# Kernel optimization log

Measured on AMD Instinct MI355X. Metric: run time of the kernel, lower is better.

## Reference

```python
import jax, jax.numpy as jnp
import numpy as np

EPS_BN = 1e-5


def conv2d(x, w, b=None, pad=0, groups=1):
    y = jax.lax.conv_general_dilated(
        x, w, window_strides=(1, 1), padding=[(pad, pad), (pad, pad)],
        dimension_numbers=('NCHW', 'OIHW', 'NCHW'), feature_group_count=groups)
    if b is not None:
        y = y + b[None, :, None, None]
    return y


def bilinear_sample(x, py, px):
    # x: (C,H,W); py,px: (T,Ho,Wo) fractional sample coords. Zero outside borders
    # (matches torchvision deform_conv2d per-corner masking).
    C, H, W = x.shape
    xf = x.reshape(C, -1)
    y0 = jnp.floor(py)
    x0 = jnp.floor(px)

    def g(yi, xi):
        valid = (yi >= 0) & (yi <= H - 1) & (xi >= 0) & (xi <= W - 1)
        idx = (jnp.clip(yi, 0, H - 1).astype(jnp.int32) * W
               + jnp.clip(xi, 0, W - 1).astype(jnp.int32))
        v = xf[:, idx.reshape(-1)].reshape((C,) + idx.shape)  # (C,T,Ho,Wo)
        return jnp.where(valid[None], v, 0.0)

    wy1 = py - y0
    wx1 = px - x0
    wy0 = 1.0 - wy1
    wx0 = 1.0 - wx1
    return (g(y0, x0) * (wy0 * wx0)[None]
            + g(y0, x0 + 1.0) * (wy0 * wx1)[None]
            + g(y0 + 1.0, x0) * (wy1 * wx0)[None]
            + g(y0 + 1.0, x0 + 1.0) * (wy1 * wx1)[None])


def deform_depthwise(x, offset, dyn_w, k):
    # x: (B,C,H,W); offset: (B,2*k*k,H,W) interleaved (dy,dx) per tap;
    # dyn_w: (B,C,k,k) per-sample depthwise kernels. stride=1, pad=k//2.
    B, C, H, W = x.shape
    T = k * k
    pad = k // 2
    off = offset.reshape(B, T, 2, H, W)
    ky, kx = jnp.meshgrid(jnp.arange(k), jnp.arange(k), indexing='ij')
    base_y = (jnp.arange(H)[None, :, None] - pad
              + ky.reshape(T)[:, None, None]).astype(x.dtype)  # (T,H,1)
    base_x = (jnp.arange(W)[None, None, :] - pad
              + kx.reshape(T)[:, None, None]).astype(x.dtype)  # (T,1,W)
    py = base_y[None] + off[:, :, 0]  # (B,T,H,W)
    px = base_x[None] + off[:, :, 1]
    v = jax.vmap(bilinear_sample)(x, py, px)  # (B,C,T,H,W)
    return jnp.einsum('bct,bcthw->bchw', dyn_w.reshape(B, C, T), v)


def reference(F_c, dec_w, dec_b, off1_w, off1_b, off2_w, off2_b,
              akg_dw_w, akg_head_w, akg_head_b, pw2_w, pw2_b,
              bn_gamma, bn_beta):
    k = 3
    Kd = 7
    B, C, H, W = F_c.shape
    R = dec_w.shape[0]

    # TargetRegionDecoupler: F_i = F * M_i + F
    M = jax.nn.softmax(conv2d(F_c, dec_w, dec_b), axis=1)  # (B,R,H,W)

    outs = []
    for i in range(R):
        F_i = F_c * (1.0 + M[:, i:i + 1])
        # OffsetGenerator
        h = jax.nn.relu(conv2d(F_i, off1_w[i], off1_b[i], pad=1))
        p_i = conv2d(h, off2_w[i], off2_b[i], pad=1)  # (B,2*k*k,H,W)
        # AdaptiveKernelGenerator (exact adaptive pool: 56 -> 7 via 8x8 mean)
        d = F_i.reshape(B, C, Kd, H // Kd, Kd, W // Kd).mean(axis=(3, 5))
        d = jax.nn.relu(conv2d(d, akg_dw_w[i], None, pad=1, groups=C))
        d = d.mean(axis=(2, 3), keepdims=True)  # AdaptiveAvgPool2d(1)
        K_i = jnp.tanh(conv2d(d, akg_head_w[i], akg_head_b[i]).reshape(B, C, k, k))
        # per-sample dynamic depthwise deformable conv
        outs.append(deform_depthwise(F_i, p_i, K_i, k))

    O = conv2d(jnp.concatenate(outs, axis=1), pw2_w, pw2_b)
    # BatchNorm2d, training-mode batch statistics
    mean = O.mean(axis=(0, 2, 3), keepdims=True)
    var = O.var(axis=(0, 2, 3), keepdims=True)
    O = (O - mean) * jax.lax.rsqrt(var + EPS_BN)
    O = O * bn_gamma[None, :, None, None] + bn_beta[None, :, None, None]
    return O


def setup_inputs() -> dict:
    key = jax.random.key(0)
    ks = jax.random.split(key, 10)
    B, C, H, W = 8, 256, 56, 56
    k, R = 3, 2
    hid = max(32, C // 4)
    return {
        'F_c': jax.random.normal(ks[0], (B, C, H, W), jnp.float32),
        'dec_w': jax.random.normal(ks[1], (R, C, 1, 1), jnp.float32) * 0.1,
        'dec_b': jnp.zeros((R,), jnp.float32),
        'off1_w': jax.random.normal(ks[2], (R, hid, C, 3, 3), jnp.float32) * 0.05,
        'off1_b': jnp.zeros((R, hid), jnp.float32),
        'off2_w': jax.random.normal(ks[3], (R, 2 * k * k, hid, 3, 3), jnp.float32) * 0.01,
        'off2_b': jnp.zeros((R, 2 * k * k), jnp.float32),
        'akg_dw_w': jax.random.normal(ks[4], (R, C, 1, 3, 3), jnp.float32) * 0.1,
        'akg_head_w': jax.random.normal(ks[5], (R, C * k * k, C, 1, 1), jnp.float32) * 0.05,
        'akg_head_b': jnp.zeros((R, C * k * k), jnp.float32),
        'pw2_w': jax.random.normal(ks[6], (C, R * C, 1, 1), jnp.float32) * 0.05,
        'pw2_b': jnp.zeros((C,), jnp.float32),
        'bn_gamma': jnp.ones((C,), jnp.float32),
        'bn_beta': jnp.zeros((C,), jnp.float32),
    }
```

## Files before the change

### kernel.cpp

```cpp
#include <hip/hip_runtime.h>
#include <hip/hip_bf16.h>

#define BB 8
#define CC_ 256
#define HH 56
#define WW 56
#define HWSZ (HH*WW)
#define RR_ 2
#define HID 64
#define FPR ((size_t)8*58*58*256)
#define HPR ((size_t)8*58*58*64)
#define NPIX ((size_t)BB*HWSZ)

typedef __hip_bfloat16 bf16;
typedef __attribute__((ext_vector_type(8))) short short8;
typedef __attribute__((ext_vector_type(4))) short short4_t;
typedef __attribute__((ext_vector_type(4))) float f32x4;

struct Tap { int o00, o01, o10, o11; float w00, w01, w10, w11; };

__device__ __forceinline__ float b2f(bf16 v){ return __bfloat162float(v); }
__device__ __forceinline__ bf16 f2b(float v){ return __float2bfloat16(v); }
__device__ __forceinline__ float bs2f(short s){ return __uint_as_float(((unsigned)(unsigned short)s)<<16); }

__global__ __launch_bounds__(256) void k_scalepack(const float* __restrict__ F, const float* __restrict__ dec_w,
                                                   const float* __restrict__ dec_b,
                                                   bf16* __restrict__ Fp, float* __restrict__ rowsum){
    __shared__ float lds_f[256][57];
    __shared__ float lw0[256], lw1[256];
    __shared__ float ls0[56], ls1[56];
    int bx = blockIdx.x; int b = bx/HH, gy = bx%HH;
    int tid = threadIdx.x;
    lw0[tid] = dec_w[tid]; lw1[tid] = dec_w[CC_+tid];
    const float* Fb = F + (size_t)b*CC_*HWSZ + gy*WW;
    for (int it = 0; it < 56; ++it){
        int idx = it*256 + tid;
        int c = idx / 56, x = idx - c*56;
        lds_f[c][x] = Fb[(size_t)c*HWSZ + x];
    }
    __syncthreads();
    if (tid < 56){
        float a0 = dec_b[0], a1 = dec_b[1];
        for (int c = 0; c < CC_; ++c){ float v = lds_f[c][tid]; a0 += v*lw0[c]; a1 += v*lw1[c]; }
        float m = fmaxf(a0,a1);
        float e0 = __expf(a0-m), e1 = __expf(a1-m);
        float inv = 1.0f/(e0+e1);
        ls0[tid] = 1.0f + e0*inv; ls1[tid] = 1.0f + e1*inv;
    }
    __syncthreads();
    bf16 z = f2b(0.f);
    for (int r = 0; r < 2; ++r){
        const float* lsr = r ? ls1 : ls0;
        bf16* slab = Fp + (size_t)r*FPR + (size_t)b*58*58*256;
        bf16* dst = slab + ((size_t)(gy+1)*58 + 1)*256 + tid;
        for (int x2 = 0; x2 < 56; ++x2) dst[(size_t)x2*256] = f2b(lds_f[tid][x2] * lsr[x2]);
        float* rs = rowsum + ((((size_t)(r*8+b)*56 + gy)*7))*256 + tid;
        #pragma unroll
        for (int v = 0; v < 7; ++v){
            float sum = 0.f;
            #pragma unroll
            for (int k = 0; k < 8; ++k) sum += lds_f[tid][v*8+k] * lsr[v*8+k];
            rs[(size_t)v*256] = sum;
        }
        bf16* rowp = slab + (size_t)(gy+1)*58*256;
        rowp[tid] = z;
        rowp[57*256 + tid] = z;
        if (gy == 0){ for (int cidx = 0; cidx < 58; ++cidx) slab[(size_t)cidx*256 + tid] = z; }
        if (gy == 55){ bf16* r57 = slab + (size_t)57*58*256;
                       for (int cidx = 0; cidx < 58; ++cidx) r57[(size_t)cidx*256 + tid] = z; }
    }
}

__global__ void k_bprep_all(const float* __restrict__ w1, const float* __restrict__ wpw,
                            const float* __restrict__ wc2,
                            bf16* __restrict__ Bp, bf16* __restrict__ Bpw, bf16* __restrict__ Bc){
    int id = blockIdx.x;
    int L = threadIdx.x;
    if (id < 576){
        int nt = id & 3; id >>= 2; int icc = id & 7; id >>= 3; int t = id % 9; int r = id / 9;
        int oc = nt*16 + (L&15);
        const float* wr = w1 + (size_t)r*HID*CC_*9;
        bf16* out = Bp + (((((size_t)r*9 + t)*8 + icc)*4 + nt)*64 + L)*8;
        #pragma unroll
        for (int j = 0; j < 8; ++j){
            int ic = icc*32 + (L>>4)*8 + j;
            out[j] = f2b(wr[((size_t)oc*CC_ + ic)*9 + t]);
        }
    } else if (id < 832){
        id -= 576;
        int kk = id >> 4, nt = id & 15;
        int oc = nt*16 + (L&15);
        bf16* out = Bpw + (((size_t)(kk*16+nt))*64 + L)*8;
        #pragma unroll
        for (int j = 0; j < 8; ++j){
            int ic = kk*32 + (L>>4)*8 + j;
            out[j] = f2b(wpw[(size_t)oc*512 + ic]);
        }
    } else {
        id -= 832;
        int nt = id & 1; id >>= 1; int ks = id % 18; int r = id / 18;
        int t = ks >> 1, chunk = ks & 1;
        int oc = nt*16 + (L&15);
        const float* wr = wc2 + (size_t)r*18*HID*9;
        bf16* out = Bc + ((((size_t)r*18 + ks)*2 + nt)*64 + L)*8;
        #pragma unroll
        for (int j = 0; j < 8; ++j){
            int ic = chunk*32 + (L>>4)*8 + j;
            out[j] = (oc < 18) ? f2b(wr[((size_t)oc*HID + ic)*9 + t]) : f2b(0.f);
        }
    }
}

__global__ __launch_bounds__(256, 1) void k_conv1(const bf16* __restrict__ Fp, const bf16* __restrict__ Bp,
                                                  const float* __restrict__ bias, bf16* __restrict__ hp){
    __shared__ __attribute__((aligned(16))) bf16 alds[4*58*264];
    __shared__ __attribute__((aligned(16))) bf16 blds[16384];
    int bx = blockIdx.x;
    int x8 = bx & 7, g = bx >> 3;
    int r = x8 >> 2;
    int b = (g/28)*4 + (x8 & 3);
    int yp = g % 28;
    int y0 = yp*2;
    int tid = threadIdx.x; int wave = tid>>6, lane = tid&63;
    int m = lane&15, q = lane>>4;
    int x0 = (wave==3) ? 40 : wave*16;
    f32x4 acc[2][4];
    #pragma unroll
    for (int i=0;i<2;++i)
        #pragma unroll
        for (int j=0;j<4;++j) acc[i][j] = (f32x4){0,0,0,0};
    const bf16* Fb = Fp + (size_t)r*FPR + ((size_t)b*58*58)*256;
    const bf16* Bpr = Bp + (size_t)r*9*16384;
    short8 pf[8];
    #pragma unroll
    for (int j = 0; j < 8; ++j) pf[j] = *(const short8*)(Bpr + (size_t)(j*256 + tid)*8);
    const bf16* FbA = Fb + (size_t)y0*58*256;
    for (int kb = 0; kb < 4; ++kb){
        short8 v[8];
        #pragma unroll
        for (int j = 0; j < 8; ++j){
            int k = kb*8 + j;
            if (k < 29) v[j] = *(const short8*)(FbA + (size_t)k*2048 + tid*8);
        }
        #pragma unroll
        for (int j = 0; j < 8; ++j){
            int k = kb*8 + j;
            if (k < 29){
                int e = k*2048 + tid*8;
                int xl = e >> 8, c = e & 255;
                int row = xl / 58, x = xl - row*58;
                *(short8*)&alds[row*15312 + x*264 + c] = v[j];
            }
        }
    }
    #pragma unroll 1
    for (int t = 0; t < 9; ++t){
        __syncthreads();
        #pragma unroll
        for (int j = 0; j < 8; ++j) *(short8*)&blds[(j*256 + tid)*8] = pf[j];
        __syncthreads();
        if (t < 8){
            const bf16* src = Bpr + (size_t)(t+1)*16384;
            #pragma unroll
            for (int j = 0; j < 8; ++j) pf[j] = *(const short8*)(src + (size_t)(j*256 + tid)*8);
        }
        int ty = t/3, tx = t%3;
        int abase = ty*15312 + (x0+m+tx)*264 + q*8;
        #pragma unroll
        for (int icc = 0; icc < 8; ++icc){
            short8 a0 = *(const short8*)&alds[abase + icc*32];
            short8 a1 = *(const short8*)&alds[abase + 15312 + icc*32];
            const bf16* bb = &blds[icc*2048 + lane*8];
            short8 b0 = *(const short8*)(bb);
            short8 b1 = *(const short8*)(bb + 512);
            short8 b2 = *(const short8*)(bb + 1024);
            short8 b3 = *(const short8*)(bb + 1536);
            acc[0][0] = __builtin_amdgcn_mfma_f32_16x16x32_bf16(a0, b0, acc[0][0], 0, 0, 0);
            acc[1][0] = __builtin_amdgcn_mfma_f32_16x16x32_bf16(a1, b0, acc[1][0], 0, 0, 0);
            acc[0][1] = __builtin_amdgcn_mfma_f32_16x16x32_bf16(a0, b1, acc[0][1], 0, 0, 0);
            acc[1][1] = __builtin_amdgcn_mfma_f32_16x16x32_bf16(a1, b1, acc[1][1], 0, 0, 0);
            acc[0][2] = __builtin_amdgcn_mfma_f32_16x16x32_bf16(a0, b2, acc[0][2], 0, 0, 0);
            acc[1][2] = __builtin_amdgcn_mfma_f32_16x16x32_bf16(a1, b2, acc[1][2], 0, 0, 0);
            acc[0][3] = __builtin_amdgcn_mfma_f32_16x16x32_bf16(a0, b3, acc[0][3], 0, 0, 0);
            acc[1][3] = __builtin_amdgcn_mfma_f32_16x16x32_bf16(a1, b3, acc[1][3], 0, 0, 0);
        }
    }
    const float* br = bias + r*HID;
    bf16* slab = hp + (size_t)r*HPR + (size_t)b*58*58*64;
    bf16 z = f2b(0.f);
    #pragma unroll
    for (int rr = 0; rr < 2; ++rr){
        int y = y0 + rr;
        bf16* hrow = slab + ((size_t)(y+1)*58 + 1)*64;
        #pragma unroll
        for (int nt = 0; nt < 4; ++nt){
            int oc = nt*16 + m;
            float bv = br[oc];
            #pragma unroll
            for (int r2 = 0; r2 < 4; ++r2){
                int x = x0 + q*4 + r2;
                hrow[(size_t)x*64 + oc] = f2b(fmaxf(acc[rr][nt][r2] + bv, 0.f));
            }
        }
        bf16* rowp = slab + (size_t)(y+1)*58*64;
        if (tid < 64) rowp[tid] = z;
        else if (tid < 128) rowp[57*64 + (tid-64)] = z;
        if (y == 0){ for (int idx = tid; idx < 58*64; idx += 256) slab[idx] = z; }
        if (y == 55){ bf16* r57 = slab + (size_t)57*58*64;
                      for (int idx = tid; idx < 58*64; idx += 256) r57[idx] = z; }
    }
}

__global__ __launch_bounds__(256) void k_conv2m(const bf16* __restrict__ hp, const bf16* __restrict__ Bc,
                                                const float* __restrict__ bias, Tap* __restrict__ tap){
    __shared__ float pld[18][56];
    int bx = blockIdx.x; int b = bx & 7; int rid = bx >> 3; int y = rid % 56; int r = rid / 56;
    int tid = threadIdx.x; int wave = tid>>6, lane = tid&63;
    int m = lane&15, q = lane>>4;
    int x0 = (wave==3) ? 40 : wave*16;
    f32x4 acc0 = {0,0,0,0}, acc1 = {0,0,0,0};
    const bf16* Hb = hp + (size_t)r*HPR + ((size_t)b*58 + y)*58*64;
    const bf16* Bcr = Bc + (size_t)r*18*2*64*8;
    #pragma unroll
    for (int t = 0; t < 9; ++t){
        int ty = t/3, tx = t%3;
        const bf16* arow = Hb + ((size_t)ty*58 + (x0+m+tx))*64 + q*8;
        #pragma unroll
        for (int chunk = 0; chunk < 2; ++chunk){
            short8 a = *(const short8*)(arow + chunk*32);
            const bf16* bb = Bcr + (((size_t)(t*2+chunk))*2*64 + lane)*8;
            short8 b0 = *(const short8*)(bb);
            short8 b1 = *(const short8*)(bb + 64*8);
            acc0 = __builtin_amdgcn_mfma_f32_16x16x32_bf16(a, b0, acc0, 0, 0, 0);
            acc1 = __builtin_amdgcn_mfma_f32_16x16x32_bf16(a, b1, acc1, 0, 0, 0);
        }
    }
    const float* br = bias + r*18;
    #pragma unroll
    for (int r2 = 0; r2 < 4; ++r2){
        int x = x0 + q*4 + r2;
        pld[m][x] = acc0[r2] + br[m];
        if (m < 2) pld[16+m][x] = acc1[r2] + br[16+m];
    }
    __syncthreads();
    for (int e = tid; e < 504; e += 256){
        int t = e / 56, x = e % 56;
        int ky = t / 3, kx = t % 3;
        float dy = pld[2*t][x];
        float dx = pld[2*t+1][x];
        float py = (float)(y - 1 + ky) + dy;
        float px = (float)(x - 1 + kx) + dx;
        float y0f = floorf(py), x0f = floorf(px);
        float wy1 = py - y0f, wx1 = px - x0f;
        float wy0 = 1.f - wy1, wx0 = 1.f - wx1;
        float vy0 = (y0f >= 0.f  && y0f <= 55.f) ? 1.f : 0.f;
        float vy1 = (y0f >= -1.f && y0f <= 54.f) ? 1.f : 0.f;
        float vx0 = (x0f >= 0.f  && x0f <= 55.f) ? 1.f : 0.f;
        float vx1 = (x0f >= -1.f && x0f <= 54.f) ? 1.f : 0.f;
        int yy0 = (int)y0f, x0i = (int)x0f;
        int iy0 = min(max(yy0,0),55),   iy1 = min(max(yy0+1,0),55);
        int ix0 = min(max(x0i,0),55),   ix1 = min(max(x0i+1,0),55);
        Tap td;
        td.o00 = ((iy0+1)*58 + ix0+1)*256;
        td.o01 = ((iy0+1)*58 + ix1+1)*256;
        td.o10 = ((iy1+1)*58 + ix0+1)*256;
        td.o11 = ((iy1+1)*58 + ix1+1)*256;
        td.w00 = wy0*wx0*vy0*vx0;
        td.w01 = wy0*wx1*vy0*vx1;
        td.w10 = wy1*wx0*vy1*vx0;
        td.w11 = wy1*wx1*vy1*vx1;
        size_t pid = ((size_t)(r*8 + b))*3136 + y*56 + x;
        tap[pid*9 + t] = td;
    }
}

__global__ __launch_bounds__(256) void k_akg_s(const float* __restrict__ rowsum, const float* __restrict__ dw,
                                               float* __restrict__ s){
    int rb = blockIdx.x; int r = rb >> 3;
    int c = threadIdx.x;
    const float* rs = rowsum + ((size_t)rb*56*7)*256 + c;
    float d[7][7];
    #pragma unroll
    for (int u = 0; u < 7; ++u)
        #pragma unroll
        for (int v = 0; v < 7; ++v){
            float acc = 0.f;
            #pragma unroll
            for (int k = 0; k < 8; ++k) acc += rs[(size_t)((u*8+k)*7 + v)*256];
            d[u][v] = acc * (1.f/64.f);
        }
    const float* wp = dw + (size_t)r*CC_*9 + c*9;
    float w[9];
    #pragma unroll
    for (int k = 0; k < 9; ++k) w[k] = wp[k];
    float tot = 0.f;
    #pragma unroll
    for (int u = 0; u < 7; ++u)
        #pragma unroll
        for (int v = 0; v < 7; ++v){
            float acc = 0.f;
            #pragma unroll
            for (int ky = 0; ky < 3; ++ky){
                int uu = u+ky-1; if ((unsigned)uu >= 7u) continue;
                #pragma unroll
                for (int kx = 0; kx < 3; ++kx){
                    int vv = v+kx-1; if ((unsigned)vv >= 7u) continue;
                    acc += d[uu][vv]*w[ky*3+kx];
                }
            }
            tot += fmaxf(acc, 0.f);
        }
    s[(size_t)rb*CC_ + c] = tot * (1.f/49.f);
}

__global__ void k_akg_head(const float* __restrict__ s, const float* __restrict__ hw,
                           const float* __restrict__ hb, float* __restrict__ Kw){
    int gid = blockIdx.x; int r = gid / 72; int id = gid % 72;
    int b = id / 9; int og = id % 9;
    __shared__ float sv[CC_];
    int tid = threadIdx.x;
    sv[tid] = s[(size_t)(r*8+b)*CC_ + tid];
    __syncthreads();
    int o = og*256 + tid;
    const float* wp = hw + (size_t)r*2304*CC_ + (size_t)o*CC_;
    float acc = hb[(size_t)r*2304 + o];
    for (int c2=0;c2<CC_;++c2) acc += wp[c2]*sv[c2];
    int c = o / 9, t = o - 9*c;
    Kw[((size_t)r*BB + b)*2304 + t*256 + c] = tanhf(acc);
}

__global__ __launch_bounds__(256, 8) void k_deform(const bf16* __restrict__ Fp, const Tap* __restrict__ tap,
                                                   const float* __restrict__ Kw, bf16* __restrict__ outsN){
    __shared__ float klds[2432];
    __shared__ Tap tlds[4][18];
    int bx = blockIdx.x; int b = bx & 7; int rest = bx >> 3;
    int pg = rest % 392; int creg = rest / 392;
    int tid = threadIdx.x; int w = tid >> 6, l = tid & 63;
    int wu = __builtin_amdgcn_readfirstlane(w);
    int yx0 = pg*8 + wu*2;
    size_t slab = (size_t)(creg*8 + b)*3136;
    const float* Kb = Kw + ((size_t)creg*8 + b)*2304;
    for (int i = tid*4; i < 2304; i += 1024){
        f32x4 v = *(const f32x4*)(Kb + i);
        int t = i >> 8, rem = i & 255;
        *(f32x4*)&klds[(rem >> 3)*76 + t*8 + (rem & 4)] = v;
    }
    if (l < 36)
        *(f32x4*)((char*)&tlds[wu][0] + l*16) =
            *(const f32x4*)((const char*)(tap + (slab + yx0)*9) + l*16);
    __syncthreads();
    int h = l >> 5, li = l & 31;
    const bf16* Fb = Fp + (size_t)creg*FPR + (size_t)b*58*58*256;
    int c0 = li*8;
    const float* kl = &klds[li*76];
    const Tap* tw = &tlds[wu][h*9];
    float acc[8];
    #pragma unroll
    for (int j = 0; j < 8; ++j) acc[j] = 0.f;
    #pragma unroll 3
    for (int t = 0; t < 9; ++t){
        Tap d = tw[t];
        short8 f00 = *(const short8*)(Fb + d.o00 + c0);
        short8 f01 = *(const short8*)(Fb + d.o01 + c0);
        short8 f10 = *(const short8*)(Fb + d.o10 + c0);
        short8 f11 = *(const short8*)(Fb + d.o11 + c0);
        f32x4 klo = *(const f32x4*)(kl + t*8);
        f32x4 khi = *(const f32x4*)(kl + t*8 + 4);
        #pragma unroll
        for (int j = 0; j < 4; ++j){
            float v = d.w00*bs2f(f00[j]) + d.w01*bs2f(f01[j]) + d.w10*bs2f(f10[j]) + d.w11*bs2f(f11[j]);
            acc[j] += klo[j]*v;
        }
        #pragma unroll
        for (int j = 4; j < 8; ++j){
            float v = d.w00*bs2f(f00[j]) + d.w01*bs2f(f01[j]) + d.w10*bs2f(f10[j]) + d.w11*bs2f(f11[j]);
            acc[j] += khi[j-4]*v;
        }
    }
    __attribute__((aligned(16))) bf16 tmp[8];
    #pragma unroll
    for (int j = 0; j < 8; ++j) tmp[j] = f2b(acc[j]);
    *(short8*)(outsN + ((size_t)b*HWSZ + yx0 + h)*512 + creg*256 + c0) = *(const short8*)tmp;
}

__global__ __launch_bounds__(256) void k_pw2_mstats(const bf16* __restrict__ outsN, const bf16* __restrict__ Bpw,
                                                    const float* __restrict__ bias, float* __restrict__ stats,
                                                    float* __restrict__ O){
    __shared__ float ls[2][2][256];
    int tid = threadIdx.x; int wave = tid>>6, lane = tid&63;
    int pixGroup = wave>>1, ntH = wave&1;
    int m = lane&15, q = lane>>4;
    size_t pb = (size_t)blockIdx.x*64 + pixGroup*32;
    const bf16* Ap0 = outsN + (pb + m)*512 + q*8;
    const bf16* Ap1 = Ap0 + (size_t)16*512;
    f32x4 acc[2][8];
    #pragma unroll
    for (int g=0;g<2;++g)
        #pragma unroll
        for (int i=0;i<8;++i) acc[g][i] = (f32x4){0,0,0,0};
    #pragma unroll 1
    for (int kk = 0; kk < 16; ++kk){
        short8 a0 = *(const short8*)(Ap0 + kk*32);
        short8 a1 = *(const short8*)(Ap1 + kk*32);
        const bf16* Bk = Bpw + (((size_t)kk*16 + ntH*8)*64 + lane)*8;
        #pragma unroll
        for (int nt2 = 0; nt2 < 8; ++nt2){
            short8 b = *(const short8*)(Bk + (size_t)nt2*64*8);
            acc[0][nt2] = __builtin_amdgcn_mfma_f32_16x16x32_bf16(a0, b, acc[0][nt2], 0, 0, 0);
            acc[1][nt2] = __builtin_amdgcn_mfma_f32_16x16x32_bf16(a1, b, acc[1][nt2], 0, 0, 0);
        }
    }
    #pragma unroll
    for (int nt2 = 0; nt2 < 8; ++nt2){
        int oc = ntH*128 + nt2*16 + m;
        float bv = bias[oc];
        float s1 = 0.f, s2 = 0.f;
        #pragma unroll
        for (int g = 0; g < 2; ++g){
            size_t pbg = pb + g*16;
            int b_idx = (int)(pbg / HWSZ);
            int yx0 = (int)(pbg % HWSZ);
            float* op = O + ((size_t)b_idx*CC_ + oc)*HWSZ + yx0 + q*4;
            #pragma unroll
            for (int r = 0; r < 4; ++r){
                float v = acc[g][nt2][r] + bv;
                op[r] = v;
                s1 += v; s2 += v*v;
            }
        }
        s1 += __shfl_down(s1, 32); s1 += __shfl_down(s1, 16);
        s2 += __shfl_down(s2, 32); s2 += __shfl_down(s2, 16);
        if (q == 0){ ls[pixGroup][0][oc] = s1; ls[pixGroup][1][oc] = s2; }
    }
    __syncthreads();
    if (tid < 256){
        atomicAdd(&stats[tid],       ls[0][0][tid] + ls[1][0][tid]);
        atomicAdd(&stats[256 + tid], ls[0][1][tid] + ls[1][1][tid]);
    }
}

__global__ __launch_bounds__(256) void k_bnapply(const float* __restrict__ O, const float* __restrict__ stats,
                                                 const float* __restrict__ gamma, const float* __restrict__ beta,
                                                 float* __restrict__ out){
    int n = (blockIdx.x*256 + threadIdx.x)*4;
    int c = (n / HWSZ) % CC_;
    float ninv = 1.f/(float)NPIX;
    float mean = stats[c]*ninv;
    float var = fmaxf(stats[256+c]*ninv - mean*mean, 0.f);
    float rsq = rsqrtf(var + 1e-5f);
    float g = gamma[c], be = beta[c];
    f32x4 v = *(const f32x4*)(O + n);
    f32x4 o;
    #pragma unroll
    for (int j = 0; j < 4; ++j) o[j] = (v[j] - mean)*rsq*g + be;
    *(f32x4*)(out + n) = o;
}

extern "C" void kernel_launch(void* const* d_in, const int* in_sizes, int n_in,
                              void* d_out, int out_size, void* d_ws, size_t ws_size,
                              hipStream_t stream) {
    (void)in_sizes; (void)n_in; (void)out_size; (void)ws_size;
    const float* F_c    = (const float*)d_in[0];
    const float* dec_w  = (const float*)d_in[1];
    const float* dec_b  = (const float*)d_in[2];
    const float* off1_w = (const float*)d_in[3];
    const float* off1_b = (const float*)d_in[4];
    const float* off2_w = (const float*)d_in[5];
    const float* off2_b = (const float*)d_in[6];
    const float* akg_dw = (const float*)d_in[7];
    const float* akg_hw = (const float*)d_in[8];
    const float* akg_hb = (const float*)d_in[9];
    const float* pw2_w  = (const float*)d_in[10];
    const float* pw2_b  = (const float*)d_in[11];
    const float* gamma  = (const float*)d_in[12];
    const float* beta   = (const float*)d_in[13];
    float* out = (float*)d_out;

    char* ws = (char*)d_ws;
    size_t off = 0;
    auto alloc = [&](size_t bytes)->char*{
        char* r = ws + off;
        off = (off + bytes + 255) & ~(size_t)255;
        return r;
    };
    bf16*  Fp    = (bf16*) alloc(2*FPR*2);
    bf16*  Bp    = (bf16*) alloc((size_t)2*9*16384*2);
    bf16*  Bpw   = (bf16*) alloc((size_t)16*16*64*8*2);
    bf16*  Bc    = (bf16*) alloc((size_t)2*18*2*64*8*2);
    float* rowsum= (float*)alloc((size_t)2*8*56*7*256*4);
    bf16*  hp    = (bf16*) alloc(2*HPR*2);
    float* s     = (float*)alloc((size_t)2*BB*CC_*4);
    float* Kw    = (float*)alloc((size_t)2*BB*CC_*9*4);
    bf16*  outsN = (bf16*) alloc(NPIX*512*2);
    Tap*   tap   = (Tap*)  alloc((size_t)2*NPIX*9*sizeof(Tap));
    float* stats = (float*)alloc(2*CC_*4);
    float* O = (float*)Fp;

    hipMemsetAsync(stats, 0, 2*CC_*sizeof(float), stream);

    k_scalepack<<<dim3(BB*HH), dim3(256), 0, stream>>>(F_c, dec_w, dec_b, Fp, rowsum);
    k_bprep_all<<<dim3(904), dim3(64), 0, stream>>>(off1_w, pw2_w, off2_w, Bp, Bpw, Bc);

    k_conv1<<<dim3(2*BB*28), dim3(256), 0, stream>>>(Fp, Bp, off1_b, hp);
    k_conv2m<<<dim3(2*BB*HH), dim3(256), 0, stream>>>(hp, Bc, off2_b, tap);
    k_akg_s<<<dim3(16), dim3(256), 0, stream>>>(rowsum, akg_dw, s);
    k_akg_head<<<dim3(2*BB*9), dim3(256), 0, stream>>>(s, akg_hw, akg_hb, Kw);
    k_deform<<<dim3(2*BB*392), dim3(256), 0, stream>>>(Fp, tap, Kw, outsN);

    k_pw2_mstats<<<dim3(392), dim3(256), 0, stream>>>(outsN, Bpw, pw2_b, stats, O);
    k_bnapply<<<dim3((int)(NPIX*CC_/1024)), dim3(256), 0, stream>>>(O, stats, gamma, beta, out);
}
```

Measured before the change: 255.0 us.

## Merge weight-prep and AKG kernels into scalepack and conv1 launches

Folds the weight-packing kernel into extra blocks of the scalepack launch, and folds the AKG pooling/depthwise and head-projection kernels into extra blocks of the conv1 launch. This removes three kernel launches and lets the small independent work run concurrently with larger kernels. The AKG head now runs in just 16 blocks, each looping over 9 output groups, instead of 144 blocks. That lowers its parallelism, and those blocks may become the tail of the conv1 launch.

New measurement: 290.5 us. 1.14x slower.

```diff
diff --git a/kernel.cpp b/kernel.cpp
--- a/kernel.cpp
+++ b/kernel.cpp
@@ -25,12 +25,55 @@
 
 __global__ __launch_bounds__(256) void k_scalepack(const float* __restrict__ F, const float* __restrict__ dec_w,
                                                    const float* __restrict__ dec_b,
-                                                   bf16* __restrict__ Fp, float* __restrict__ rowsum){
+                                                   bf16* __restrict__ Fp, float* __restrict__ rowsum,
+                                                   const float* __restrict__ w1, const float* __restrict__ wpw,
+                                                   const float* __restrict__ wc2,
+                                                   bf16* __restrict__ Bp, bf16* __restrict__ Bpw,
+                                                   bf16* __restrict__ Bc){
     __shared__ float lds_f[256][57];
     __shared__ float lw0[256], lw1[256];
     __shared__ float ls0[56], ls1[56];
-    int bx = blockIdx.x; int b = bx/HH, gy = bx%HH;
+    int bx = blockIdx.x;
     int tid = threadIdx.x;
+    if (bx >= 448){
+        int id = (bx - 448)*4 + (tid >> 6);
+        int L = tid & 63;
+        if (id < 576){
+            int nt = id & 3; id >>= 2; int icc = id & 7; id >>= 3; int t = id % 9; int r = id / 9;
+            int oc = nt*16 + (L&15);
+            const float* wr = w1 + (size_t)r*HID*CC_*9;
+            bf16* out = Bp + (((((size_t)r*9 + t)*8 + icc)*4 + nt)*64 + L)*8;
+            #pragma unroll
+            for (int j = 0; j < 8; ++j){
+                int ic = icc*32 + (L>>4)*8 + j;
+                out[j] = f2b(wr[((size_t)oc*CC_ + ic)*9 + t]);
+            }
+        } else if (id < 832){
+            id -= 576;
+            int kk = id >> 4, nt = id & 15;
+            int oc = nt*16 + (L&15);
+            bf16* out = Bpw + (((size_t)(kk*16+nt))*64 + L)*8;
+            #pragma unroll
+            for (int j = 0; j < 8; ++j){
+                int ic = kk*32 + (L>>4)*8 + j;
+                out[j] = f2b(wpw[(size_t)oc*512 + ic]);
+            }
+        } else if (id < 904){
+            id -= 832;
+            int nt = id & 1; id >>= 1; int ks = id % 18; int r = id / 18;
+            int t = ks >> 1, chunk = ks & 1;
+            int oc = nt*16 + (L&15);
+            const float* wr = wc2 + (size_t)r*18*HID*9;
+            bf16* out = Bc + ((((size_t)r*18 + ks)*2 + nt)*64 + L)*8;
+            #pragma unroll
+            for (int j = 0; j < 8; ++j){
+                int ic = chunk*32 + (L>>4)*8 + j;
+                out[j] = (oc < 18) ? f2b(wr[((size_t)oc*HID + ic)*9 + t]) : f2b(0.f);
+            }
+        }
+        return;
+    }
+    int b = bx/HH, gy = bx%HH;
     lw0[tid] = dec_w[tid]; lw1[tid] = dec_w[CC_+tid];
     const float* Fb = F + (size_t)b*CC_*HWSZ + gy*WW;
     for (int it = 0; it < 56; ++it){
@@ -71,57 +114,71 @@
     }
 }
 
-__global__ void k_bprep_all(const float* __restrict__ w1, const float* __restrict__ wpw,
-                            const float* __restrict__ wc2,
-                            bf16* __restrict__ Bp, bf16* __restrict__ Bpw, bf16* __restrict__ Bc){
-    int id = blockIdx.x;
-    int L = threadIdx.x;
-    if (id < 576){
-        int nt = id & 3; id >>= 2; int icc = id & 7; id >>= 3; int t = id % 9; int r = id / 9;
-        int oc = nt*16 + (L&15);
-        const float* wr = w1 + (size_t)r*HID*CC_*9;
-        bf16* out = Bp + (((((size_t)r*9 + t)*8 + icc)*4 + nt)*64 + L)*8;
-        #pragma unroll
-        for (int j = 0; j < 8; ++j){
-            int ic = icc*32 + (L>>4)*8 + j;
-            out[j] = f2b(wr[((size_t)oc*CC_ + ic)*9 + t]);
-        }
-    } else if (id < 832){
-        id -= 576;
-        int kk = id >> 4, nt = id & 15;
-        int oc = nt*16 + (L&15);
-        bf16* out = Bpw + (((size_t)(kk*16+nt))*64 + L)*8;
-        #pragma unroll
-        for (int j = 0; j < 8; ++j){
-            int ic = kk*32 + (L>>4)*8 + j;
-            out[j] = f2b(wpw[(size_t)oc*512 + ic]);
-        }
-    } else {
-        id -= 832;
-        int nt = id & 1; id >>= 1; int ks = id % 18; int r = id / 18;
-        int t = ks >> 1, chunk = ks & 1;
-        int oc = nt*16 + (L&15);
-        const float* wr = wc2 + (size_t)r*18*HID*9;
-        bf16* out = Bc + ((((size_t)r*18 + ks)*2 + nt)*64 + L)*8;
-        #pragma unroll
-        for (int j = 0; j < 8; ++j){
-            int ic = chunk*32 + (L>>4)*8 + j;
-            out[j] = (oc < 18) ? f2b(wr[((size_t)oc*HID + ic)*9 + t]) : f2b(0.f);
-        }
-    }
-}
-
 __global__ __launch_bounds__(256, 1) void k_conv1(const bf16* __restrict__ Fp, const bf16* __restrict__ Bp,
-                                                  const float* __restrict__ bias, bf16* __restrict__ hp){
+                                                  const float* __restrict__ bias, bf16* __restrict__ hp,
+                                                  const float* __restrict__ rowsum, const float* __restrict__ dw,
+                                                  const float* __restrict__ hw, const float* __restrict__ hb,
+                                                  float* __restrict__ Kw){
     __shared__ __attribute__((aligned(16))) bf16 alds[4*58*264];
     __shared__ __attribute__((aligned(16))) bf16 blds[16384];
     int bx = blockIdx.x;
+    int tid = threadIdx.x;
+    if (bx >= 448){
+        int rb = bx - 448; int r = rb >> 3;
+        int c = tid;
+        float* sv = (float*)alds;
+        const float* rs = rowsum + ((size_t)rb*56*7)*256 + c;
+        float d[7][7];
+        #pragma unroll
+        for (int u = 0; u < 7; ++u)
+            #pragma unroll
+            for (int v = 0; v < 7; ++v){
+                float acc = 0.f;
+                #pragma unroll
+                for (int k = 0; k < 8; ++k) acc += rs[(size_t)((u*8+k)*7 + v)*256];
+                d[u][v] = acc * (1.f/64.f);
+            }
+        const float* wp = dw + (size_t)r*CC_*9 + c*9;
+        float w[9];
+        #pragma unroll
+        for (int k = 0; k < 9; ++k) w[k] = wp[k];
+        float tot = 0.f;
+        #pragma unroll
+        for (int u = 0; u < 7; ++u)
+            #pragma unroll
+            for (int v = 0; v < 7; ++v){
+                float acc = 0.f;
+                #pragma unroll
+                for (int ky = 0; ky < 3; ++ky){
+                    int uu = u+ky-1; if ((unsigned)uu >= 7u) continue;
+                    #pragma unroll
+                    for (int kx = 0; kx < 3; ++kx){
+                        int vv = v+kx-1; if ((unsigned)vv >= 7u) continue;
+                        acc += d[uu][vv]*w[ky*3+kx];
+                    }
+                }
+                tot += fmaxf(acc, 0.f);
+            }
+        sv[c] = tot * (1.f/49.f);
+        __syncthreads();
+        int b = rb & 7;
+        #pragma unroll
+        for (int og = 0; og < 9; ++og){
+            int o = og*256 + tid;
+            const float* hwp = hw + (size_t)r*2304*CC_ + (size_t)o*CC_;
+            float acc = hb[(size_t)r*2304 + o];
+            for (int c2 = 0; c2 < CC_; ++c2) acc += hwp[c2]*sv[c2];
+            int cc = o / 9, t = o - 9*cc;
+            Kw[((size_t)r*BB + b)*2304 + t*256 + cc] = tanhf(acc);
+        }
+        return;
+    }
     int x8 = bx & 7, g = bx >> 3;
     int r = x8 >> 2;
     int b = (g/28)*4 + (x8 & 3);
     int yp = g % 28;
     int y0 = yp*2;
-    int tid = threadIdx.x; int wave = tid>>6, lane = tid&63;
+    int wave = tid>>6, lane = tid&63;
     int m = lane&15, q = lane>>4;
     int x0 = (wave==3) ? 40 : wave*16;
     f32x4 acc[2][4];
@@ -274,61 +331,6 @@
     }
 }
 
-__global__ __launch_bounds__(256) void k_akg_s(const float* __restrict__ rowsum, const float* __restrict__ dw,
-                                               float* __restrict__ s){
-    int rb = blockIdx.x; int r = rb >> 3;
-    int c = threadIdx.x;
-    const float* rs = rowsum + ((size_t)rb*56*7)*256 + c;
-    float d[7][7];
-    #pragma unroll
-    for (int u = 0; u < 7; ++u)
-        #pragma unroll
-        for (int v = 0; v < 7; ++v){
-            float acc = 0.f;
-            #pragma unroll
-            for (int k = 0; k < 8; ++k) acc += rs[(size_t)((u*8+k)*7 + v)*256];
-            d[u][v] = acc * (1.f/64.f);
-        }
-    const float* wp = dw + (size_t)r*CC_*9 + c*9;
-    float w[9];
-    #pragma unroll
-    for (int k = 0; k < 9; ++k) w[k] = wp[k];
-    float tot = 0.f;
-    #pragma unroll
-    for (int u = 0; u < 7; ++u)
-        #pragma unroll
-        for (int v = 0; v < 7; ++v){
-            float acc = 0.f;
-            #pragma unroll
-            for (int ky = 0; ky < 3; ++ky){
-                int uu = u+ky-1; if ((unsigned)uu >= 7u) continue;
-                #pragma unroll
-                for (int kx = 0; kx < 3; ++kx){
-                    int vv = v+kx-1; if ((unsigned)vv >= 7u) continue;
-                    acc += d[uu][vv]*w[ky*3+kx];
-                }
-            }
-            tot += fmaxf(acc, 0.f);
-        }
-    s[(size_t)rb*CC_ + c] = tot * (1.f/49.f);
-}
-
-__global__ void k_akg_head(const float* __restrict__ s, const float* __restrict__ hw,
-                           const float* __restrict__ hb, float* __restrict__ Kw){
-    int gid = blockIdx.x; int r = gid / 72; int id = gid % 72;
-    int b = id / 9; int og = id % 9;
-    __shared__ float sv[CC_];
-    int tid = threadIdx.x;
-    sv[tid] = s[(size_t)(r*8+b)*CC_ + tid];
-    __syncthreads();
-    int o = og*256 + tid;
-    const float* wp = hw + (size_t)r*2304*CC_ + (size_t)o*CC_;
-    float acc = hb[(size_t)r*2304 + o];
-    for (int c2=0;c2<CC_;++c2) acc += wp[c2]*sv[c2];
-    int c = o / 9, t = o - 9*c;
-    Kw[((size_t)r*BB + b)*2304 + t*256 + c] = tanhf(acc);
-}
-
 __global__ __launch_bounds__(256, 8) void k_deform(const bf16* __restrict__ Fp, const Tap* __restrict__ tap,
                                                    const float* __restrict__ Kw, bf16* __restrict__ outsN){
     __shared__ float klds[2432];
@@ -489,7 +491,6 @@
     bf16*  Bc    = (bf16*) alloc((size_t)2*18*2*64*8*2);
     float* rowsum= (float*)alloc((size_t)2*8*56*7*256*4);
     bf16*  hp    = (bf16*) alloc(2*HPR*2);
-    float* s     = (float*)alloc((size_t)2*BB*CC_*4);
     float* Kw    = (float*)alloc((size_t)2*BB*CC_*9*4);
     bf16*  outsN = (bf16*) alloc(NPIX*512*2);
     Tap*   tap   = (Tap*)  alloc((size_t)2*NPIX*9*sizeof(Tap));
@@ -498,13 +499,11 @@
 
     hipMemsetAsync(stats, 0, 2*CC_*sizeof(float), stream);
 
-    k_scalepack<<<dim3(BB*HH), dim3(256), 0, stream>>>(F_c, dec_w, dec_b, Fp, rowsum);
-    k_bprep_all<<<dim3(904), dim3(64), 0, stream>>>(off1_w, pw2_w, off2_w, Bp, Bpw, Bc);
-
-    k_conv1<<<dim3(2*BB*28), dim3(256), 0, stream>>>(Fp, Bp, off1_b, hp);
+    k_scalepack<<<dim3(448 + 226), dim3(256), 0, stream>>>(F_c, dec_w, dec_b, Fp, rowsum,
+                                                           off1_w, pw2_w, off2_w, Bp, Bpw, Bc);
+    k_conv1<<<dim3(448 + 16), dim3(256), 0, stream>>>(Fp, Bp, off1_b, hp,
+                                                      rowsum, akg_dw, akg_hw, akg_hb, Kw);
     k_conv2m<<<dim3(2*BB*HH), dim3(256), 0, stream>>>(hp, Bc, off2_b, tap);
-    k_akg_s<<<dim3(16), dim3(256), 0, stream>>>(rowsum, akg_dw, s);
-    k_akg_head<<<dim3(2*BB*9), dim3(256), 0, stream>>>(s, akg_hw, akg_hb, Kw);
     k_deform<<<dim3(2*BB*392), dim3(256), 0, stream>>>(Fp, tap, Kw, outsN);
 
     k_pw2_mstats<<<dim3(392), dim3(256), 0, stream>>>(outsN, Bpw, pw2_b, stats, O);
```
